# Optimization experiments

Measured on AMD Instinct MI355X. Metric: run time of the kernel, lower is better.

Reference implementation:

```python
import jax, jax.numpy as jnp
import numpy as np

EPS = 1e-5
HEADS = 4
N_SIDE = 32  # im_h == im_w


def _rel_pos_indices(n):
    idx = np.arange(n)
    xi = np.repeat(idx, n)
    yi = np.tile(idx, n)
    pos = np.stack([xi, yi])                      # [2, n^2]
    d = pos[:, None, :] - pos[:, :, None]          # [2, n^2, n^2]
    d = np.clip(d, -n, n) + (n - 1)
    return d[0], d[1]


def _conv1x1(x, W):
    # x: [b,c,H,W], W: [o,c]
    return jnp.einsum('bchw,oc->bohw', x, W)


def _bn(x, g, b, m, v):
    inv = jax.lax.rsqrt(v + EPS)
    return (x - m[:, None, None]) * (inv * g)[:, None, None] + b[:, None, None]


def setup_inputs() -> dict:
    key = jax.random.key(0)
    ks = jax.random.split(key, 8)
    b, dim, H = 16, 256, N_SIDE
    dim_k, heads, dim_out = 16, HEADS, 256
    dim_v = dim_out // heads
    return {
        'x': jax.random.normal(ks[0], (b, dim, H, H), jnp.float32),
        'Wq': jax.random.normal(ks[1], (dim_k * heads, dim), jnp.float32) * 0.05,
        'Wk': jax.random.normal(ks[2], (dim_k, dim), jnp.float32) * 0.05,
        'Wv': jax.random.normal(ks[3], (dim_v, dim), jnp.float32) * 0.05,
        'gq': jnp.ones((dim_k * heads,), jnp.float32),
        'bq': jnp.zeros((dim_k * heads,), jnp.float32),
        'mq': jax.random.normal(ks[4], (dim_k * heads,), jnp.float32) * 0.1,
        'vq': jax.random.uniform(ks[5], (dim_k * heads,), jnp.float32, 0.5, 1.5),
        'gv': jnp.ones((dim_v,), jnp.float32),
        'bv': jnp.zeros((dim_v,), jnp.float32),
        'mv': jax.random.normal(ks[6], (dim_v,), jnp.float32) * 0.1,
        'vv': jax.random.uniform(ks[7], (dim_v,), jnp.float32, 0.5, 1.5),
        'rel_pos_emb': jax.random.normal(jax.random.fold_in(key, 7), (2 * H - 1, 2 * H - 1, dim_k), jnp.float32) * 0.05,
    }


def reference(x, Wq, Wk, Wv, gq, bq, mq, vq, gv, bv, mv, vv, rel_pos_emb):
    b, c, H, W = x.shape
    heads = HEADS
    m = H * W
    dim_k = Wk.shape[0]
    dim_v = Wv.shape[0]

    Q = _bn(_conv1x1(x, Wq), gq, bq, mq, vq)              # [b, h*k, H, W]
    K = _conv1x1(x, Wk)                                   # [b, k, H, W]
    V = _bn(_conv1x1(x, Wv), gv, bv, mv, vv)              # [b, v, H, W]

    Q = Q.reshape(b, heads, dim_k, m).transpose(0, 1, 3, 2)   # [b, h, m, k]
    K = K.reshape(b, dim_k, m).transpose(0, 2, 1)             # [b, m, k]
    V = V.reshape(b, dim_v, m).transpose(0, 2, 1)             # [b, m, v]

    sK = jax.nn.softmax(K, axis=-1)  # NOTE: source softmaxes over k, not m
    lam_c = jnp.einsum('bmk,bmv->bkv', sK, V)
    content = jnp.einsum('bhnk,bkv->bnhv', Q, lam_c)

    r0, r1 = _rel_pos_indices(H)
    emb = rel_pos_emb[r0, r1]                         # [m, m, k]
    lam_p = jnp.einsum('nmk,bmv->bnkv', emb, V)       # [b, m, k, v]
    position = jnp.einsum('bhnk,bnkv->bnhv', Q, lam_p)

    out = content + position                          # [b, m, h, v]
    return out.reshape(b, H, W, heads * dim_v)
```

## Files before the change

### kernel.cpp

```cpp
#include <hip/hip_runtime.h>
#include <math.h>

namespace {
typedef unsigned short u16;
typedef __attribute__((ext_vector_type(4))) float f32x4;
typedef __attribute__((ext_vector_type(8))) short bf16x8;

constexpr int kB  = 16;
constexpr int kC  = 256;
constexpr int kM  = 1024;

__device__ inline u16 f2b(float f) {
    union { float f; unsigned u; } un; un.f = f;
    unsigned r = un.u + 0x7FFF + ((un.u >> 16) & 1);
    return (u16)(r >> 16);
}
__device__ inline float b2f(u16 u) {
    union { unsigned u; float f; } un; un.u = ((unsigned)u) << 16; return un.f;
}

__global__ __launch_bounds__(256) void k_prep(
    const float* __restrict__ Wq, const float* __restrict__ Wk,
    const float* __restrict__ Wv,
    const float* __restrict__ gq, const float* __restrict__ bq,
    const float* __restrict__ mq, const float* __restrict__ vq,
    const float* __restrict__ gv, const float* __restrict__ bv,
    const float* __restrict__ mv, const float* __restrict__ vv,
    const float* __restrict__ rpe,
    u16* __restrict__ Wb, float* __restrict__ bb, u16* __restrict__ rpe_b)
{
    const int bid = blockIdx.x;
    const int t = threadIdx.x;
    if (bid < 9) {
        const int oc = bid * 16 + (t >> 4);
        const int c0 = (t & 15) * 16;
        float s, bias;
        const float* wrow;
        if (oc < 64)      { float inv = rsqrtf(vq[oc] + 1e-5f); s = inv * gq[oc]; bias = bq[oc] - mq[oc] * s; wrow = Wq + (size_t)oc * kC; }
        else if (oc < 80) { s = 1.f; bias = 0.f; wrow = Wk + (size_t)(oc - 64) * kC; }
        else              { int i2 = oc - 80; float inv = rsqrtf(vv[i2] + 1e-5f); s = inv * gv[i2]; bias = bv[i2] - mv[i2] * s; wrow = Wv + (size_t)i2 * kC; }
#pragma unroll
        for (int cc = 0; cc < 16; ++cc)
            Wb[(size_t)oc * kC + c0 + cc] = f2b(wrow[c0 + cc] * s);
        if (c0 == 0) bb[oc] = bias;
    } else {
        const int dr = bid - 9;
        for (int e = t; e < 2048; e += 256) {
            int dc = e >> 5, k = e & 31;
            float v = (dc < 63 && k < 16) ? rpe[((size_t)dr * 63 + dc) * 16 + k] : 0.f;
            rpe_b[((size_t)dr * 64 + dc) * 32 + k] = f2b(v);
        }
    }
}

__global__ __launch_bounds__(256) void k_qkv(
    const float* __restrict__ x, const u16* __restrict__ Wb,
    const float* __restrict__ bb,
    u16* __restrict__ Qb, float* __restrict__ Kf, u16* __restrict__ Vb)
{
    __shared__ float Xs[256][18];

    const int b  = blockIdx.y;
    const int m0 = blockIdx.x * 16;
    const int t  = threadIdx.x;
    const int w  = t >> 6, lane = t & 63, li = lane & 15, lg = lane >> 4;

#pragma unroll
    for (int j = 0; j < 4; ++j) {
        int e = t + 256 * j;
        int c = e >> 2, m4 = (e & 3) * 4;
        *(float4*)&Xs[c][m4] = *(const float4*)&x[(size_t)(b * kC + c) * kM + m0 + m4];
    }
    __syncthreads();

    const int nt = (w == 0) ? 3 : 2;
    const int t0 = (w == 0) ? 0 : 2 * w + 1;

    f32x4 acc[3];
#pragma unroll
    for (int i = 0; i < 3; ++i) acc[i] = (f32x4){0.f, 0.f, 0.f, 0.f};

    for (int ch = 0; ch < 8; ++ch) {
        const int c0 = ch * 32 + lg * 8;
        bf16x8 bfr;
#pragma unroll
        for (int j = 0; j < 8; ++j) bfr[j] = (short)f2b(Xs[c0 + j][li]);
        for (int i = 0; i < nt; ++i) {
            bf16x8 afr = *(const bf16x8*)&Wb[(size_t)((t0 + i) * 16 + li) * kC + c0];
            acc[i] = __builtin_amdgcn_mfma_f32_16x16x32_bf16(afr, bfr, acc[i], 0, 0, 0);
        }
    }

    const int m = m0 + li;
    for (int i = 0; i < nt; ++i) {
        const int tile = t0 + i;
        const int ocb = tile * 16 + lg * 4;
        float o[4];
#pragma unroll
        for (int reg = 0; reg < 4; ++reg) o[reg] = acc[i][reg] + bb[ocb + reg];
        if (tile < 4) {
            u16 pk[4];
#pragma unroll
            for (int reg = 0; reg < 4; ++reg) pk[reg] = f2b(o[reg]);
            u16* qp = Qb + ((size_t)(b * 4 + tile) * kM + m) * 32;
            *(uint2*)&qp[lg * 4] = *(const uint2*)pk;
            uint2 z; z.x = 0u; z.y = 0u;
            *(uint2*)&qp[16 + lg * 4] = z;
        } else if (tile == 4) {
#pragma unroll
            for (int reg = 0; reg < 4; ++reg)
                Kf[(size_t)(b * 16 + lg * 4 + reg) * kM + m] = o[reg];
        } else {
            const int vb = (tile - 5) * 16 + lg * 4;
#pragma unroll
            for (int reg = 0; reg < 4; ++reg)
                Vb[(size_t)(b * 64 + vb + reg) * kM + m] = f2b(o[reg]);
        }
    }
}

__global__ __launch_bounds__(256) void k_lam(
    const float* __restrict__ Kf, const u16* __restrict__ Vb,
    float* __restrict__ lam_parts)
{
    __shared__ float Ks[16][64];
    __shared__ float Vsh[64][69];

    const int b = blockIdx.y, mb = blockIdx.x;
    const int m0 = mb * 64;
    const int t = threadIdx.x;
    const float* Kc = Kf + (size_t)b * 16 * kM + m0;
    const u16*   Vc = Vb + (size_t)b * 64 * kM + m0;

#pragma unroll
    for (int j = 0; j < 4; ++j) {
        int e = t + 256 * j;
        Ks[e >> 6][e & 63] = Kc[(size_t)(e >> 6) * kM + (e & 63)];
    }
#pragma unroll
    for (int j = 0; j < 4; ++j) {
        int e = t + 256 * j;
        int v = e >> 4, mq = (e & 15) * 4;
        uint2 pv = *(const uint2*)&Vc[(size_t)v * kM + mq];
        u16 pp[4]; *(uint2*)pp = pv;
#pragma unroll
        for (int i = 0; i < 4; ++i) Vsh[v][mq + i] = b2f(pp[i]);
    }
    __syncthreads();

    if (t < 64) {
        float vals[16];
        float mx = -1e30f;
#pragma unroll
        for (int k = 0; k < 16; ++k) { vals[k] = Ks[k][t]; mx = fmaxf(mx, vals[k]); }
        float sum = 0.f;
#pragma unroll
        for (int k = 0; k < 16; ++k) { vals[k] = __expf(vals[k] - mx); sum += vals[k]; }
        const float inv = 1.f / sum;
#pragma unroll
        for (int k = 0; k < 16; ++k) Ks[k][t] = vals[k] * inv;
    }
    __syncthreads();

    const int v = t & 63, kq = t >> 6;
    float a[4] = {0.f, 0.f, 0.f, 0.f};
#pragma unroll 4
    for (int mm = 0; mm < 64; ++mm) {
        const float vv_ = Vsh[v][mm];
#pragma unroll
        for (int j = 0; j < 4; ++j) a[j] += Ks[kq * 4 + j][mm] * vv_;
    }
    float* o = lam_parts + (size_t)(mb * kB + b) * 1024;
#pragma unroll
    for (int j = 0; j < 4; ++j) o[(kq * 4 + j) * 64 + v] = a[j];
}

__global__ __launch_bounds__(256, 4) void k_attn(
    const u16* __restrict__ Qb, const u16* __restrict__ Vb,
    const u16* __restrict__ rpe_b, const float* __restrict__ lam_parts,
    float* __restrict__ out)
{
    __shared__ float lc[16][65];
    __shared__ u16 Sl[4][16][68];

    const int b = blockIdx.y, nblk = blockIdx.x, n0 = nblk * 16;
    const int t = threadIdx.x;
    const int h = t >> 6, lane = t & 63, li = lane & 15, lg = lane >> 4;
    const int ny = n0 >> 5;
    const int dshift = 31 - (n0 & 16);
    const int gbase = (n0 & 16) ? 0 : 1;

    const u16* Vbb = Vb + (size_t)b * 64 * kM;
    u16* Sh = &Sl[h][0][0];

    for (int e = t; e < 1024; e += 256) {
        float s = 0.f;
#pragma unroll
        for (int p = 0; p < 16; ++p) s += lam_parts[(size_t)(p * kB + b) * 1024 + e];
        lc[e >> 6][e & 63] = s;
    }

    const u16* Qbase = Qb + ((size_t)(b * 4 + h) * kM + n0) * 32;
    bf16x8 qf = *(const bf16x8*)&Qbase[(size_t)li * 32 + lg * 8];

    bf16x8 ra[3];
    {
        const int dr = 31 - ny;
#pragma unroll
        for (int g = 0; g < 3; ++g)
            ra[g] = *(const bf16x8*)&rpe_b[((size_t)dr * 64 + (gbase + g) * 16 + li) * 32 + lg * 8];
    }

    __syncthreads();

    f32x4 acc[4];
#pragma unroll
    for (int c = 0; c < 4; ++c) {
        bf16x8 cb;
#pragma unroll
        for (int j = 0; j < 8; ++j) {
            int k = lg * 8 + j;
            cb[j] = (k < 16) ? (short)f2b(lc[k][16 * c + li]) : (short)0;
        }
        f32x4 z = {0.f, 0.f, 0.f, 0.f};
        acc[c] = __builtin_amdgcn_mfma_f32_16x16x32_bf16(qf, cb, z, 0, 0, 0);
    }

    const int swr = li * 68;
    const int src0 = swr + 8 * lg + dshift - li;

#pragma unroll 2
    for (int mrow = 0; mrow < 32; ++mrow) {
        bf16x8 vf[4];
#pragma unroll
        for (int c = 0; c < 4; ++c)
            vf[c] = *(const bf16x8*)&Vbb[(size_t)(16 * c + li) * kM + mrow * 32 + lg * 8];

        f32x4 tq[3];
#pragma unroll
        for (int g = 0; g < 3; ++g) {
            f32x4 z = {0.f, 0.f, 0.f, 0.f};
            tq[g] = __builtin_amdgcn_mfma_f32_16x16x32_bf16(ra[g], qf, z, 0, 0, 0);
        }

        if (mrow < 31) {
            const int dr = mrow + 1 - ny + 31;
#pragma unroll
            for (int g = 0; g < 3; ++g)
                ra[g] = *(const bf16x8*)&rpe_b[((size_t)dr * 64 + (gbase + g) * 16 + li) * 32 + lg * 8];
        }

#pragma unroll
        for (int g = 0; g < 3; ++g) {
            u16 pk[4];
#pragma unroll
            for (int reg = 0; reg < 4; ++reg) pk[reg] = f2b(tq[g][reg]);
            *(uint2*)&Sh[swr + (gbase + g) * 16 + 4 * lg] = *(const uint2*)pk;
        }

        asm volatile("" ::: "memory");

        bf16x8 sa;
#pragma unroll
        for (int j = 0; j < 8; ++j)
            sa[j] = (short)Sh[src0 + j];

        __builtin_amdgcn_s_setprio(1);
#pragma unroll
        for (int c = 0; c < 4; ++c)
            acc[c] = __builtin_amdgcn_mfma_f32_16x16x32_bf16(sa, vf[c], acc[c], 0, 0, 0);
        __builtin_amdgcn_s_setprio(0);
    }

    float* ob = out + ((size_t)b * kM + n0) * 256 + h * 64;
#pragma unroll
    for (int c = 0; c < 4; ++c)
#pragma unroll
        for (int reg = 0; reg < 4; ++reg)
            ob[(size_t)(4 * lg + reg) * 256 + 16 * c + li] = acc[c][reg];
}

}

extern "C" void kernel_launch(void* const* d_in, const int* in_sizes, int n_in,
                              void* d_out, int out_size, void* d_ws, size_t ws_size,
                              hipStream_t stream) {
    const float* x   = (const float*)d_in[0];
    const float* Wq  = (const float*)d_in[1];
    const float* Wk  = (const float*)d_in[2];
    const float* Wv  = (const float*)d_in[3];
    const float* gq  = (const float*)d_in[4];
    const float* bq  = (const float*)d_in[5];
    const float* mq  = (const float*)d_in[6];
    const float* vq  = (const float*)d_in[7];
    const float* gv  = (const float*)d_in[8];
    const float* bv  = (const float*)d_in[9];
    const float* mv  = (const float*)d_in[10];
    const float* vv  = (const float*)d_in[11];
    const float* rpe = (const float*)d_in[12];
    float* out = (float*)d_out;

    float* Kf        = (float*)d_ws;
    float* lam_parts = Kf + (size_t)16 * 16 * 1024;
    float* bbuf      = lam_parts + (size_t)16 * 16 * 1024;
    u16*   Qb        = (u16*)(bbuf + 256);
    u16*   Vb        = Qb + (size_t)16 * 4 * 1024 * 32;
    u16*   rpe_b     = Vb + (size_t)16 * 64 * 1024;
    u16*   Wb        = rpe_b + (size_t)63 * 64 * 32;

    k_prep<<<72, 256, 0, stream>>>(Wq, Wk, Wv, gq, bq, mq, vq, gv, bv, mv, vv,
                                   rpe, Wb, bbuf, rpe_b);
    k_qkv<<<dim3(64, 16), 256, 0, stream>>>(x, Wb, bbuf, Qb, Kf, Vb);
    k_lam<<<dim3(16, 16), 256, 0, stream>>>(Kf, Vb, lam_parts);
    k_attn<<<dim3(64, 16), 256, 0, stream>>>(Qb, Vb, rpe_b, lam_parts, out);
}
```

Before: 193.5 us.

## Rework qkv staging, MFMA lambda reduction, and 32-row attention tiles

k_qkv now converts x to bf16 once while staging it transposed in shared memory, so B fragments are loaded as single vectors instead of per-element converts. k_lam becomes one block per batch that computes softmax(K)·V with MFMA and writes a bf16 lambda, which removes the 16-way partial-sum reduction that k_attn used to redo. k_attn processes 32 query rows per block, covering a full image row with all 4 rpe groups, and reuses each V fragment across two query tiles. It also prefetches the next rpe and V fragments. The cost is more registers per thread (launch bounds lowered to 2 waves), half as many attn blocks, and a k_lam grid of only 16 blocks.

```diff
diff --git a/kernel.cpp b/kernel.cpp
--- a/kernel.cpp
+++ b/kernel.cpp
@@ -14,9 +14,6 @@
     union { float f; unsigned u; } un; un.f = f;
     unsigned r = un.u + 0x7FFF + ((un.u >> 16) & 1);
     return (u16)(r >> 16);
-}
-__device__ inline float b2f(u16 u) {
-    union { unsigned u; float f; } un; un.u = ((unsigned)u) << 16; return un.f;
 }
 
 __global__ __launch_bounds__(256) void k_prep(
@@ -58,7 +55,7 @@
     const float* __restrict__ bb,
     u16* __restrict__ Qb, float* __restrict__ Kf, u16* __restrict__ Vb)
 {
-    __shared__ float Xs[256][18];
+    __shared__ u16 Xs[16][264];
 
     const int b  = blockIdx.y;
     const int m0 = blockIdx.x * 16;
@@ -69,7 +66,11 @@
     for (int j = 0; j < 4; ++j) {
         int e = t + 256 * j;
         int c = e >> 2, m4 = (e & 3) * 4;
-        *(float4*)&Xs[c][m4] = *(const float4*)&x[(size_t)(b * kC + c) * kM + m0 + m4];
+        float4 xv = *(const float4*)&x[(size_t)(b * kC + c) * kM + m0 + m4];
+        Xs[m4 + 0][c] = f2b(xv.x);
+        Xs[m4 + 1][c] = f2b(xv.y);
+        Xs[m4 + 2][c] = f2b(xv.z);
+        Xs[m4 + 3][c] = f2b(xv.w);
     }
     __syncthreads();
 
@@ -82,9 +83,7 @@
 
     for (int ch = 0; ch < 8; ++ch) {
         const int c0 = ch * 32 + lg * 8;
-        bf16x8 bfr;
-#pragma unroll
-        for (int j = 0; j < 8; ++j) bfr[j] = (short)f2b(Xs[c0 + j][li]);
+        bf16x8 bfr = *(const bf16x8*)&Xs[li][c0];
         for (int i = 0; i < nt; ++i) {
             bf16x8 afr = *(const bf16x8*)&Wb[(size_t)((t0 + i) * 16 + li) * kC + c0];
             acc[i] = __builtin_amdgcn_mfma_f32_16x16x32_bf16(afr, bfr, acc[i], 0, 0, 0);
@@ -119,165 +118,156 @@
     }
 }
 
-__global__ __launch_bounds__(256) void k_lam(
+__global__ __launch_bounds__(512) void k_lam(
     const float* __restrict__ Kf, const u16* __restrict__ Vb,
-    float* __restrict__ lam_parts)
+    u16* __restrict__ lamb)
 {
-    __shared__ float Ks[16][64];
-    __shared__ float Vsh[64][69];
-
-    const int b = blockIdx.y, mb = blockIdx.x;
-    const int m0 = mb * 64;
-    const int t = threadIdx.x;
-    const float* Kc = Kf + (size_t)b * 16 * kM + m0;
-    const u16*   Vc = Vb + (size_t)b * 64 * kM + m0;
-
-#pragma unroll
-    for (int j = 0; j < 4; ++j) {
-        int e = t + 256 * j;
-        Ks[e >> 6][e & 63] = Kc[(size_t)(e >> 6) * kM + (e & 63)];
-    }
-#pragma unroll
-    for (int j = 0; j < 4; ++j) {
-        int e = t + 256 * j;
-        int v = e >> 4, mq = (e & 15) * 4;
-        uint2 pv = *(const uint2*)&Vc[(size_t)v * kM + mq];
-        u16 pp[4]; *(uint2*)pp = pv;
-#pragma unroll
-        for (int i = 0; i < 4; ++i) Vsh[v][mq + i] = b2f(pp[i]);
-    }
-    __syncthreads();
-
-    if (t < 64) {
+    __shared__ u16 sk[16][1048];
+    __shared__ float red[2][4][16][16];
+
+    const int b = blockIdx.x, t = threadIdx.x;
+
+#pragma unroll
+    for (int j = 0; j < 2; ++j) {
+        const int m = t + 512 * j;
         float vals[16];
         float mx = -1e30f;
 #pragma unroll
-        for (int k = 0; k < 16; ++k) { vals[k] = Ks[k][t]; mx = fmaxf(mx, vals[k]); }
+        for (int k = 0; k < 16; ++k) { vals[k] = Kf[(size_t)(b * 16 + k) * kM + m]; mx = fmaxf(mx, vals[k]); }
         float sum = 0.f;
 #pragma unroll
         for (int k = 0; k < 16; ++k) { vals[k] = __expf(vals[k] - mx); sum += vals[k]; }
         const float inv = 1.f / sum;
 #pragma unroll
-        for (int k = 0; k < 16; ++k) Ks[k][t] = vals[k] * inv;
+        for (int k = 0; k < 16; ++k) sk[k][m] = f2b(vals[k] * inv);
     }
     __syncthreads();
 
-    const int v = t & 63, kq = t >> 6;
-    float a[4] = {0.f, 0.f, 0.f, 0.f};
-#pragma unroll 4
-    for (int mm = 0; mm < 64; ++mm) {
-        const float vv_ = Vsh[v][mm];
-#pragma unroll
-        for (int j = 0; j < 4; ++j) a[j] += Ks[kq * 4 + j][mm] * vv_;
-    }
-    float* o = lam_parts + (size_t)(mb * kB + b) * 1024;
-#pragma unroll
-    for (int j = 0; j < 4; ++j) o[(kq * 4 + j) * 64 + v] = a[j];
-}
-
-__global__ __launch_bounds__(256, 4) void k_attn(
+    const int w = t >> 6, lane = t & 63, li = lane & 15, lg = lane >> 4;
+    const int ms = w >> 2, vt = w & 3;
+    f32x4 acc = {0.f, 0.f, 0.f, 0.f};
+    for (int ck = 0; ck < 16; ++ck) {
+        const int mch = ms * 512 + ck * 32 + lg * 8;
+        bf16x8 af = *(const bf16x8*)&sk[li][mch];
+        bf16x8 bf_ = *(const bf16x8*)&Vb[(size_t)(b * 64 + vt * 16 + li) * kM + mch];
+        acc = __builtin_amdgcn_mfma_f32_16x16x32_bf16(af, bf_, acc, 0, 0, 0);
+    }
+#pragma unroll
+    for (int reg = 0; reg < 4; ++reg)
+        red[ms][vt][lg * 4 + reg][li] = acc[reg];
+    __syncthreads();
+
+    for (int e = t; e < 2048; e += 512) {
+        int v = e >> 5, k = e & 31;
+        u16 o = 0;
+        if (k < 16) o = f2b(red[0][v >> 4][k][v & 15] + red[1][v >> 4][k][v & 15]);
+        lamb[(size_t)b * 2048 + v * 32 + k] = o;
+    }
+}
+
+__global__ __launch_bounds__(256, 2) void k_attn(
     const u16* __restrict__ Qb, const u16* __restrict__ Vb,
-    const u16* __restrict__ rpe_b, const float* __restrict__ lam_parts,
+    const u16* __restrict__ rpe_b, const u16* __restrict__ lamb,
     float* __restrict__ out)
 {
-    __shared__ float lc[16][65];
-    __shared__ u16 Sl[4][16][68];
-
-    const int b = blockIdx.y, nblk = blockIdx.x, n0 = nblk * 16;
+    __shared__ u16 Sl[4][32][72];
+
+    const int b = blockIdx.y, nblk = blockIdx.x, n0 = nblk * 32;
     const int t = threadIdx.x;
     const int h = t >> 6, lane = t & 63, li = lane & 15, lg = lane >> 4;
-    const int ny = n0 >> 5;
-    const int dshift = 31 - (n0 & 16);
-    const int gbase = (n0 & 16) ? 0 : 1;
 
     const u16* Vbb = Vb + (size_t)b * 64 * kM;
     u16* Sh = &Sl[h][0][0];
 
-    for (int e = t; e < 1024; e += 256) {
-        float s = 0.f;
-#pragma unroll
-        for (int p = 0; p < 16; ++p) s += lam_parts[(size_t)(p * kB + b) * 1024 + e];
-        lc[e >> 6][e & 63] = s;
-    }
-
     const u16* Qbase = Qb + ((size_t)(b * 4 + h) * kM + n0) * 32;
-    bf16x8 qf = *(const bf16x8*)&Qbase[(size_t)li * 32 + lg * 8];
-
-    bf16x8 ra[3];
+    bf16x8 qf[2];
+    qf[0] = *(const bf16x8*)&Qbase[(size_t)li * 32 + lg * 8];
+    qf[1] = *(const bf16x8*)&Qbase[(size_t)(16 + li) * 32 + lg * 8];
+
+    f32x4 acc[2][4];
+    const u16* lb = lamb + (size_t)b * 2048;
+#pragma unroll
+    for (int c = 0; c < 4; ++c) {
+        bf16x8 cb = *(const bf16x8*)&lb[(size_t)(16 * c + li) * 32 + lg * 8];
+        f32x4 z = {0.f, 0.f, 0.f, 0.f};
+        acc[0][c] = __builtin_amdgcn_mfma_f32_16x16x32_bf16(qf[0], cb, z, 0, 0, 0);
+        acc[1][c] = __builtin_amdgcn_mfma_f32_16x16x32_bf16(qf[1], cb, z, 0, 0, 0);
+    }
+
+    bf16x8 ra[4], vf[4];
     {
-        const int dr = 31 - ny;
-#pragma unroll
-        for (int g = 0; g < 3; ++g)
-            ra[g] = *(const bf16x8*)&rpe_b[((size_t)dr * 64 + (gbase + g) * 16 + li) * 32 + lg * 8];
-    }
-
-    __syncthreads();
-
-    f32x4 acc[4];
-#pragma unroll
-    for (int c = 0; c < 4; ++c) {
-        bf16x8 cb;
-#pragma unroll
-        for (int j = 0; j < 8; ++j) {
-            int k = lg * 8 + j;
-            cb[j] = (k < 16) ? (short)f2b(lc[k][16 * c + li]) : (short)0;
-        }
-        f32x4 z = {0.f, 0.f, 0.f, 0.f};
-        acc[c] = __builtin_amdgcn_mfma_f32_16x16x32_bf16(qf, cb, z, 0, 0, 0);
-    }
-
-    const int swr = li * 68;
-    const int src0 = swr + 8 * lg + dshift - li;
+        const int dr = 31 - nblk;
+#pragma unroll
+        for (int g = 0; g < 4; ++g)
+            ra[g] = *(const bf16x8*)&rpe_b[((size_t)dr * 64 + g * 16 + li) * 32 + lg * 8];
+#pragma unroll
+        for (int c = 0; c < 4; ++c)
+            vf[c] = *(const bf16x8*)&Vbb[(size_t)(16 * c + li) * kM + lg * 8];
+    }
 
 #pragma unroll 2
     for (int mrow = 0; mrow < 32; ++mrow) {
-        bf16x8 vf[4];
+        bf16x8 ran[4], vfn[4];
+        if (mrow < 31) {
+            const int dr = mrow + 1 - nblk + 31;
+            const int mb2 = (mrow + 1) * 32;
+#pragma unroll
+            for (int g = 0; g < 4; ++g)
+                ran[g] = *(const bf16x8*)&rpe_b[((size_t)dr * 64 + g * 16 + li) * 32 + lg * 8];
+#pragma unroll
+            for (int c = 0; c < 4; ++c)
+                vfn[c] = *(const bf16x8*)&Vbb[(size_t)(16 * c + li) * kM + mb2 + lg * 8];
+        }
+
+        f32x4 tq[4][2];
+#pragma unroll
+        for (int g = 0; g < 4; ++g) {
+            f32x4 z = {0.f, 0.f, 0.f, 0.f};
+            tq[g][0] = __builtin_amdgcn_mfma_f32_16x16x32_bf16(ra[g], qf[0], z, 0, 0, 0);
+            tq[g][1] = __builtin_amdgcn_mfma_f32_16x16x32_bf16(ra[g], qf[1], z, 0, 0, 0);
+        }
+
+#pragma unroll
+        for (int g = 0; g < 4; ++g)
+#pragma unroll
+            for (int r = 0; r < 2; ++r) {
+                u16 pk[4];
+#pragma unroll
+                for (int reg = 0; reg < 4; ++reg) pk[reg] = f2b(tq[g][r][reg]);
+                *(uint2*)&Sh[(size_t)(16 * r + li) * 72 + 16 * g + 4 * lg] = *(const uint2*)pk;
+            }
+
+        asm volatile("" ::: "memory");
+
+#pragma unroll
+        for (int r = 0; r < 2; ++r) {
+            const int base = (16 * r + li) * 72 + 8 * lg + 31 - 16 * r - li;
+            bf16x8 sa;
+#pragma unroll
+            for (int j = 0; j < 8; ++j) sa[j] = (short)Sh[base + j];
+            __builtin_amdgcn_s_setprio(1);
+#pragma unroll
+            for (int c = 0; c < 4; ++c)
+                acc[r][c] = __builtin_amdgcn_mfma_f32_16x16x32_bf16(sa, vf[c], acc[r][c], 0, 0, 0);
+            __builtin_amdgcn_s_setprio(0);
+        }
+
+        if (mrow < 31) {
+#pragma unroll
+            for (int g = 0; g < 4; ++g) ra[g] = ran[g];
+#pragma unroll
+            for (int c = 0; c < 4; ++c) vf[c] = vfn[c];
+        }
+    }
+
+    float* ob = out + ((size_t)b * kM + n0) * 256 + h * 64;
+#pragma unroll
+    for (int r = 0; r < 2; ++r)
 #pragma unroll
         for (int c = 0; c < 4; ++c)
-            vf[c] = *(const bf16x8*)&Vbb[(size_t)(16 * c + li) * kM + mrow * 32 + lg * 8];
-
-        f32x4 tq[3];
-#pragma unroll
-        for (int g = 0; g < 3; ++g) {
-            f32x4 z = {0.f, 0.f, 0.f, 0.f};
-            tq[g] = __builtin_amdgcn_mfma_f32_16x16x32_bf16(ra[g], qf, z, 0, 0, 0);
-        }
-
-        if (mrow < 31) {
-            const int dr = mrow + 1 - ny + 31;
-#pragma unroll
-            for (int g = 0; g < 3; ++g)
-                ra[g] = *(const bf16x8*)&rpe_b[((size_t)dr * 64 + (gbase + g) * 16 + li) * 32 + lg * 8];
-        }
-
-#pragma unroll
-        for (int g = 0; g < 3; ++g) {
-            u16 pk[4];
-#pragma unroll
-            for (int reg = 0; reg < 4; ++reg) pk[reg] = f2b(tq[g][reg]);
-            *(uint2*)&Sh[swr + (gbase + g) * 16 + 4 * lg] = *(const uint2*)pk;
-        }
-
-        asm volatile("" ::: "memory");
-
-        bf16x8 sa;
-#pragma unroll
-        for (int j = 0; j < 8; ++j)
-            sa[j] = (short)Sh[src0 + j];
-
-        __builtin_amdgcn_s_setprio(1);
-#pragma unroll
-        for (int c = 0; c < 4; ++c)
-            acc[c] = __builtin_amdgcn_mfma_f32_16x16x32_bf16(sa, vf[c], acc[c], 0, 0, 0);
-        __builtin_amdgcn_s_setprio(0);
-    }
-
-    float* ob = out + ((size_t)b * kM + n0) * 256 + h * 64;
-#pragma unroll
-    for (int c = 0; c < 4; ++c)
-#pragma unroll
-        for (int reg = 0; reg < 4; ++reg)
-            ob[(size_t)(4 * lg + reg) * 256 + 16 * c + li] = acc[c][reg];
+#pragma unroll
+            for (int reg = 0; reg < 4; ++reg)
+                ob[(size_t)(16 * r + 4 * lg + reg) * 256 + 16 * c + li] = acc[r][c][reg];
 }
 
 }
@@ -300,17 +290,17 @@
     const float* rpe = (const float*)d_in[12];
     float* out = (float*)d_out;
 
-    float* Kf        = (float*)d_ws;
-    float* lam_parts = Kf + (size_t)16 * 16 * 1024;
-    float* bbuf      = lam_parts + (size_t)16 * 16 * 1024;
-    u16*   Qb        = (u16*)(bbuf + 256);
-    u16*   Vb        = Qb + (size_t)16 * 4 * 1024 * 32;
-    u16*   rpe_b     = Vb + (size_t)16 * 64 * 1024;
-    u16*   Wb        = rpe_b + (size_t)63 * 64 * 32;
+    float* Kf    = (float*)d_ws;
+    float* bbuf  = Kf + (size_t)16 * 16 * 1024;
+    u16*   Qb    = (u16*)(bbuf + 256);
+    u16*   Vb    = Qb + (size_t)16 * 4 * 1024 * 32;
+    u16*   rpe_b = Vb + (size_t)16 * 64 * 1024;
+    u16*   Wb    = rpe_b + (size_t)63 * 64 * 32;
+    u16*   lamb  = Wb + (size_t)144 * 256;
 
     k_prep<<<72, 256, 0, stream>>>(Wq, Wk, Wv, gq, bq, mq, vq, gv, bv, mv, vv,
                                    rpe, Wb, bbuf, rpe_b);
     k_qkv<<<dim3(64, 16), 256, 0, stream>>>(x, Wb, bbuf, Qb, Kf, Vb);
-    k_lam<<<dim3(16, 16), 256, 0, stream>>>(Kf, Vb, lam_parts);
-    k_attn<<<dim3(64, 16), 256, 0, stream>>>(Qb, Vb, rpe_b, lam_parts, out);
-}
+    k_lam<<<16, 512, 0, stream>>>(Kf, Vb, lamb);
+    k_attn<<<dim3(32, 16), 256, 0, stream>>>(Qb, Vb, rpe_b, lamb, out);
+}
```

Result: faster. 162.2 us (-16.2%).
